# Kernel tuning notes

Measured on AMD Instinct MI355X. Metric: run time of the kernel, lower is better.

Reference implementation:

```python
import jax, jax.numpy as jnp
import numpy as np

N = 100000      # nodes
E = 3200000     # edges per graph (pos and neg)
IN_FEATS = 128
HIDDEN = 32
PROP_STEP = 8
USE_RELU = False  # args.relu default False


def setup_inputs() -> dict:
    key = jax.random.key(0)
    ks = jax.random.split(key, 8)
    in_feat = jax.random.normal(ks[0], (N, IN_FEATS), dtype=jnp.float32)
    src = jax.random.randint(ks[1], (E,), 0, N, dtype=jnp.int32)
    dst = jax.random.randint(ks[2], (E,), 0, N, dtype=jnp.int32)
    neg_src = jax.random.randint(ks[3], (E,), 0, N, dtype=jnp.int32)
    neg_dst = jax.random.randint(ks[4], (E,), 0, N, dtype=jnp.int32)
    W1 = jax.random.normal(ks[5], (IN_FEATS, HIDDEN), dtype=jnp.float32) * (1.0 / np.sqrt(IN_FEATS))
    b1 = jnp.zeros((HIDDEN,), dtype=jnp.float32)
    gamma = jnp.ones((HIDDEN,), dtype=jnp.float32)
    beta = jnp.zeros((HIDDEN,), dtype=jnp.float32)
    W2 = jax.random.normal(ks[6], (HIDDEN, HIDDEN), dtype=jnp.float32) * (1.0 / np.sqrt(HIDDEN))
    b2 = jnp.zeros((HIDDEN,), dtype=jnp.float32)
    return dict(in_feat=in_feat, W1=W1, b1=b1, gamma=gamma, beta=beta,
                W2=W2, b2=b2, src=src, dst=dst, neg_src=neg_src, neg_dst=neg_dst)


def _graph_conv(h, src, dst, n_nodes):
    """DGL GraphConv(norm='both', weight=False, bias=False):
       out = D_dst^{-1/2} A D_src^{-1/2} h, sum aggregation."""
    ones = jnp.ones(src.shape, dtype=h.dtype)
    out_deg = jax.ops.segment_sum(ones, src, num_segments=n_nodes)
    in_deg = jax.ops.segment_sum(ones, dst, num_segments=n_nodes)
    hs = h * jax.lax.rsqrt(jnp.clip(out_deg, 1.0))[:, None]   # [N, H]
    msg = hs[src]                                             # [E, H] gather
    agg = jax.ops.segment_sum(msg, dst, num_segments=n_nodes)  # [N, H] scatter-add
    return agg * jax.lax.rsqrt(jnp.clip(in_deg, 1.0))[:, None]


def reference(in_feat, W1, b1, gamma, beta, W2, b2, src, dst, neg_src, neg_dst):
    # MLP: Linear -> BatchNorm1d (training-mode batch stats) -> (Dropout noop) -> ReLU -> Linear
    x = in_feat @ W1 + b1
    mu = jnp.mean(x, axis=0)
    var = jnp.var(x, axis=0)
    x = (x - mu) * jax.lax.rsqrt(var + 1e-5) * gamma + beta
    x = jax.nn.relu(x)
    ori_h = x @ W2 + b2                                       # [N, H]

    # Iterative pos-neg SpMM propagation with residual (h initialized to ori_h)
    h = ori_h
    for _ in range(PROP_STEP):
        if USE_RELU:
            h = jax.nn.relu(h)
        h = _graph_conv(h, src, dst, N) - _graph_conv(h, neg_src, neg_dst, N) + ori_h
    return h
```

## Files before the change

### kernel.cpp

```cpp
#include <hip/hip_runtime.h>
#include <hip/hip_fp16.h>

#define N_NODES 100000
#define E_EDGES 3200000
#define IN_F 128
#define HID 32
#define PROP 8

#define WIN 32768
#define NWIN 4
#define HS 32

#define MB_ROWS 64
#define MB_BLOCKS ((N_NODES + MB_ROWS - 1) / MB_ROWS)
#define RED_B 32

#define FB 512
#define CH 12500
#define BK_SH 7
#define BK_N 128
#define NBK 782
#define L2S (NBK * FB)
#define SCB2 391
#define SPLIT 4
#define SUBN 32
#define STG 3072

__global__ __launch_bounds__(256) void hist_kernel(const int* __restrict__ s,
        const int* __restrict__ ns, int* __restrict__ degs) {
    __shared__ int lh[WIN];
    int b = blockIdx.x;
    int w = b % NWIN;
    int st = (b / NWIN) % 2;
    int sl = b / (NWIN * 2);
    const int* p = st ? ns : s;
    for (int i = threadIdx.x; i < WIN; i += 256) lh[i] = 0;
    __syncthreads();
    const int lo = w * WIN;
    const int per = E_EDGES / HS;
    const int4* p4 = (const int4*)(p + sl * per);
    for (int i = threadIdx.x; i < per / 4; i += 256) {
        int4 v = p4[i];
        int a;
        a = v.x - lo; if ((unsigned)a < WIN) atomicAdd(&lh[a], 1);
        a = v.y - lo; if ((unsigned)a < WIN) atomicAdd(&lh[a], 1);
        a = v.z - lo; if ((unsigned)a < WIN) atomicAdd(&lh[a], 1);
        a = v.w - lo; if ((unsigned)a < WIN) atomicAdd(&lh[a], 1);
    }
    __syncthreads();
    int* g = degs + st * N_NODES;
    for (int i = threadIdx.x; i < WIN; i += 256) {
        int idx = lo + i;
        if (idx < N_NODES && lh[i]) atomicAdd(&g[idx], lh[i]);
    }
}

__global__ void inv_sqrt_kernel(const int* __restrict__ deg, float* __restrict__ inv, int n) {
    int i = blockIdx.x * blockDim.x + threadIdx.x;
    if (i < n) inv[i] = rsqrtf(fmaxf((float)deg[i], 1.0f));
}

__global__ __launch_bounds__(256) void countA_kernel(const int* __restrict__ dst,
        const int* __restrict__ ndst, int* __restrict__ counts) {
    __shared__ int lh[NBK];
    int blk = blockIdx.x;
    for (int i = threadIdx.x; i < NBK; i += 256) lh[i] = 0;
    __syncthreads();
    const int* dp = (blk < FB / 2) ? dst + blk * CH : ndst + (blk - FB / 2) * CH;
    const int4* dp4 = (const int4*)dp;
    for (int i = threadIdx.x; i < CH / 4; i += 256) {
        int4 v = dp4[i];
        atomicAdd(&lh[v.x >> BK_SH], 1);
        atomicAdd(&lh[v.y >> BK_SH], 1);
        atomicAdd(&lh[v.z >> BK_SH], 1);
        atomicAdd(&lh[v.w >> BK_SH], 1);
    }
    __syncthreads();
    for (int b = threadIdx.x; b < NBK; b += 256) counts[b * FB + blk] = lh[b];
}

__global__ __launch_bounds__(1024) void scanA2_kernel(const int* __restrict__ counts,
        int* __restrict__ offs, int* __restrict__ blockSums) {
    __shared__ int sh[1024];
    int t = threadIdx.x, b = blockIdx.x;
    int i = b * 1024 + t;
    int v = counts[i];
    sh[t] = v;
    __syncthreads();
    for (int off = 1; off < 1024; off <<= 1) {
        int u = (t >= off) ? sh[t - off] : 0;
        __syncthreads();
        sh[t] += u;
        __syncthreads();
    }
    offs[i] = sh[t] - v;
    if (t == 1023) blockSums[b] = sh[1023];
}

__global__ __launch_bounds__(512) void scanB2_kernel(const int* __restrict__ blockSums,
        int* __restrict__ blockOff) {
    __shared__ int sh[512];
    int t = threadIdx.x;
    int v = (t < SCB2) ? blockSums[t] : 0;
    sh[t] = v;
    __syncthreads();
    for (int off = 1; off < 512; off <<= 1) {
        int u = (t >= off) ? sh[t - off] : 0;
        __syncthreads();
        sh[t] += u;
        __syncthreads();
    }
    if (t < SCB2) blockOff[t] = sh[t] - v;
}

__global__ __launch_bounds__(1024) void scanC2_kernel(int* __restrict__ offs,
        const int* __restrict__ blockOff) {
    int b = blockIdx.x, t = threadIdx.x;
    int i = b * 1024 + t;
    offs[i] += blockOff[b];
    if (i == 0) offs[L2S] = 2 * E_EDGES;
}

__global__ __launch_bounds__(256) void fillA2_kernel(const int* __restrict__ src, const int* __restrict__ dst,
        const int* __restrict__ nsrc, const int* __restrict__ ndst,
        const int* __restrict__ offs, int* __restrict__ rec) {
    __shared__ int cur[NBK];
    __shared__ int base[NBK];
    int blk = blockIdx.x;
    int g = (blk >= FB / 2);
    const int* sp = g ? (nsrc + (blk - FB / 2) * CH) : (src + blk * CH);
    const int* dp = g ? (ndst + (blk - FB / 2) * CH) : (dst + blk * CH);
    const int gbit = g << 24;
    for (int i = threadIdx.x; i < NBK; i += 256) {
        cur[i] = 0;
        base[i] = offs[i * FB + blk];
    }
    __syncthreads();
    for (int i = threadIdx.x; i < CH; i += 256) {
        int u = sp[i], v = dp[i];
        int b = v >> BK_SH;
        int p = base[b] + atomicAdd(&cur[b], 1);
        rec[p] = u | ((v & (BK_N - 1)) << 17) | gbit;
    }
}

__global__ __launch_bounds__(256, 5) void reorder_kernel(const int* __restrict__ offs,
        const int* __restrict__ rec, const float* __restrict__ invs,
        int2* __restrict__ rec2, int* __restrict__ row_ptr2) {
    __shared__ int cnt[BK_N];
    __shared__ int cntp[BK_N];
    __shared__ int scn[BK_N];
    __shared__ int ex[BK_N];
    __shared__ float invp[BK_N], invn[BK_N];
    __shared__ int2 stage[STG];
    int blk = blockIdx.x;
    int bkt = blk >> 2, sub = blk & (SPLIT - 1);
    int tid = threadIdx.x;
    if (tid < BK_N) { cnt[tid] = 0; cntp[tid] = 0; }
    __syncthreads();
    int beg = offs[bkt * FB], end = offs[(bkt + 1) * FB];
    for (int i = beg + tid; i < end; i += 256) {
        int rx = rec[i];
        int d = (rx >> 17) & (BK_N - 1);
        atomicAdd(&cnt[d], 1);
        if (!(rx & (1 << 24))) atomicAdd(&cntp[d], 1);
    }
    __syncthreads();
    int v = (tid < BK_N) ? cnt[tid] : 0;
    if (tid < BK_N) {
        scn[tid] = v;
        int np = cntp[tid];
        invp[tid] = rsqrtf(fmaxf((float)np, 1.0f));
        invn[tid] = rsqrtf(fmaxf((float)(v - np), 1.0f));
    }
    __syncthreads();
    for (int off = 1; off < BK_N; off <<= 1) {
        int u = (tid < BK_N && tid >= off) ? scn[tid - off] : 0;
        __syncthreads();
        if (tid < BK_N) scn[tid] += u;
        __syncthreads();
    }
    int lo = sub * SUBN, hi = lo + SUBN;
    if (tid < BK_N) {
        ex[tid] = scn[tid] - v;
        cnt[tid] = 0;
        if (tid >= lo && tid < hi)
            row_ptr2[bkt * BK_N + tid] = beg + ex[tid];
    }
    if (bkt == NBK - 1 && sub == SPLIT - 1 && tid == 0)
        row_ptr2[NBK * BK_N] = 2 * E_EDGES;
    __syncthreads();
    int base0 = ex[lo];
    int base1 = (sub == SPLIT - 1) ? (end - beg) : ex[hi];
    for (int i = beg + tid; i < end; i += 256) {
        int rx = rec[i];
        int d = (rx >> 17) & (BK_N - 1);
        if (d < lo || d >= hi) continue;
        int g = (rx >> 24) & 1;
        int u = rx & 0x1FFFF;
        float io = invs[u + (g ? N_NODES : 0)];
        float c = (g ? -io : io) * (g ? invn[d] : invp[d]);
        int p = ex[d] - base0 + atomicAdd(&cnt[d], 1);
        stage[p] = make_int2(u, __float_as_int(c));
    }
    __syncthreads();
    int n = base1 - base0;
    for (int j = tid; j < n; j += 256) rec2[beg + base0 + j] = stage[j];
}

__global__ __launch_bounds__(256) void mlp1_kernel(const float* __restrict__ in_feat,
        const float* __restrict__ W1, const float* __restrict__ b1,
        float* __restrict__ x, float* __restrict__ partials) {
    __shared__ float4 sRow4[MB_ROWS * 32];
    __shared__ float  sW1t[32 * 132];
    int tid = threadIdx.x;
    for (int idx = tid; idx < IN_F * HID; idx += 256) {
        int j = idx >> 5, k = idx & 31;
        sW1t[k * 132 + j] = W1[idx];
    }
    int nb = blockIdx.x * MB_ROWS;
    const float4* inf4 = (const float4*)in_feat;
    for (int idx = tid; idx < MB_ROWS * 32; idx += 256) {
        int row = idx >> 5, q = idx & 31;
        int g = nb + row;
        float4 v = (g < N_NODES) ? inf4[(size_t)g * 32 + q] : make_float4(0.f, 0.f, 0.f, 0.f);
        sRow4[row * 32 + (q ^ (row & 31))] = v;
    }
    __syncthreads();
    int rt = tid & 31, kt = tid >> 5;
    int k0 = kt * 4;
    float acc[2][4] = {{0.f}};
    const float4* w0p = (const float4*)&sW1t[(k0 + 0) * 132];
    const float4* w1p = (const float4*)&sW1t[(k0 + 1) * 132];
    const float4* w2p = (const float4*)&sW1t[(k0 + 2) * 132];
    const float4* w3p = (const float4*)&sW1t[(k0 + 3) * 132];
    #pragma unroll 4
    for (int jq = 0; jq < 32; ++jq) {
        int pq = jq ^ rt;
        float4 a0 = sRow4[rt * 32 + pq];
        float4 a1 = sRow4[(rt + 32) * 32 + pq];
        float4 w0 = w0p[jq], w1 = w1p[jq], w2 = w2p[jq], w3 = w3p[jq];
        acc[0][0] += a0.x*w0.x + a0.y*w0.y + a0.z*w0.z + a0.w*w0.w;
        acc[0][1] += a0.x*w1.x + a0.y*w1.y + a0.z*w1.z + a0.w*w1.w;
        acc[0][2] += a0.x*w2.x + a0.y*w2.y + a0.z*w2.z + a0.w*w2.w;
        acc[0][3] += a0.x*w3.x + a0.y*w3.y + a0.z*w3.z + a0.w*w3.w;
        acc[1][0] += a1.x*w0.x + a1.y*w0.y + a1.z*w0.z + a1.w*w0.w;
        acc[1][1] += a1.x*w1.x + a1.y*w1.y + a1.z*w1.z + a1.w*w1.w;
        acc[1][2] += a1.x*w2.x + a1.y*w2.y + a1.z*w2.z + a1.w*w2.w;
        acc[1][3] += a1.x*w3.x + a1.y*w3.y + a1.z*w3.z + a1.w*w3.w;
    }
    float bb[4] = { b1[k0], b1[k0 + 1], b1[k0 + 2], b1[k0 + 3] };
    float s[4] = {0.f, 0.f, 0.f, 0.f}, ss[4] = {0.f, 0.f, 0.f, 0.f};
    #pragma unroll
    for (int i = 0; i < 2; ++i) {
        int row = nb + rt + 32 * i;
        if (row < N_NODES) {
            float4 o;
            o.x = acc[i][0] + bb[0];
            o.y = acc[i][1] + bb[1];
            o.z = acc[i][2] + bb[2];
            o.w = acc[i][3] + bb[3];
            *(float4*)&x[(size_t)row * HID + k0] = o;
            s[0] += o.x; ss[0] += o.x * o.x;
            s[1] += o.y; ss[1] += o.y * o.y;
            s[2] += o.z; ss[2] += o.z * o.z;
            s[3] += o.w; ss[3] += o.w * o.w;
        }
    }
    for (int off = 16; off; off >>= 1) {
        #pragma unroll
        for (int c = 0; c < 4; ++c) {
            s[c]  += __shfl_down(s[c],  off, 32);
            ss[c] += __shfl_down(ss[c], off, 32);
        }
    }
    if (rt == 0) {
        float* pb = partials + (size_t)blockIdx.x * 64;
        #pragma unroll
        for (int c = 0; c < 4; ++c) {
            pb[k0 + c]      = s[c];
            pb[32 + k0 + c] = ss[c];
        }
    }
}

__global__ __launch_bounds__(256) void bnred_kernel(const float* __restrict__ partials,
        float* __restrict__ partials2) {
    __shared__ float red[4][64];
    int t = threadIdx.x, b = blockIdx.x;
    int r = t >> 6, c = t & 63;
    float sum = 0.f;
    for (int g = b * 4 + r; g < MB_BLOCKS; g += RED_B * 4)
        sum += partials[(size_t)g * 64 + c];
    red[r][c] = sum;
    __syncthreads();
    if (t < 64) partials2[b * 64 + t] = (red[0][t] + red[1][t]) + (red[2][t] + red[3][t]);
}

__global__ __launch_bounds__(256) void bnparam_kernel(const float* __restrict__ partials2,
        const float* __restrict__ gamma, const float* __restrict__ beta, float* __restrict__ params) {
    __shared__ float red[4][64];
    int t = threadIdx.x;
    int col = t & 63, ch = t >> 6;
    float sum = 0.f;
    for (int g = ch; g < RED_B; g += 4) sum += partials2[(size_t)g * 64 + col];
    red[ch][col] = sum;
    __syncthreads();
    if (t < 64) red[0][t] = red[0][t] + red[1][t] + red[2][t] + red[3][t];
    __syncthreads();
    if (t < HID) {
        float mu  = red[0][t] * (1.0f / (float)N_NODES);
        float var = red[0][t + 32] * (1.0f / (float)N_NODES) - mu * mu;
        float sg = gamma[t] * rsqrtf(var + 1e-5f);
        params[t]       = sg;
        params[HID + t] = beta[t] - mu * sg;
    }
}

__global__ __launch_bounds__(256) void mlp2_kernel(const float* __restrict__ x,
        const float* __restrict__ params, const float* __restrict__ W2,
        const float* __restrict__ b2, float* __restrict__ ori_h, __half* __restrict__ h16) {
    __shared__ float sW2[HID * HID];
    __shared__ float sXn[8][HID];
    int tid = threadIdx.x;
    for (int i = tid; i < HID * HID; i += 256) sW2[i] = W2[i];
    int nb = blockIdx.x * 8;
    int k = tid & 31, r = tid >> 5;
    float v = x[(size_t)(nb + r) * HID + k];
    v = fmaxf(fmaf(v, params[k], params[HID + k]), 0.f);
    sXn[r][k] = v;
    __syncthreads();
    float acc = b2[k];
    #pragma unroll
    for (int j = 0; j < HID; ++j) acc = fmaf(sXn[r][j], sW2[j * HID + k], acc);
    int o = (nb + r) * HID + k;
    ori_h[o] = acc;
    h16[o] = __float2half(acc);
}

__device__ __forceinline__ float2 h2f(int b) {
    __half2 h; __builtin_memcpy(&h, &b, 4); return __half22float2(h);
}

__global__ __launch_bounds__(256) void gather_kernel(const int* __restrict__ row_ptr,
        const int2* __restrict__ rec, const int4* __restrict__ h4,
        const float4* __restrict__ ori4, int4* __restrict__ hn4, float4* __restrict__ out4) {
    int tid = threadIdx.x;
    int node = blockIdx.x * 8 + (tid >> 5);
    int lane = tid & 31;
    int slot = lane >> 2;
    int ql = lane & 3;
    int beg = row_ptr[node], end = row_ptr[node + 1];
    float2 a0 = {0.f, 0.f}, a1 = {0.f, 0.f}, a2 = {0.f, 0.f}, a3 = {0.f, 0.f};
    int i = beg;
#define ACC8(f, c) { float2 u_; \
        u_ = h2f((f).x); a0.x = fmaf((c), u_.x, a0.x); a0.y = fmaf((c), u_.y, a0.y); \
        u_ = h2f((f).y); a1.x = fmaf((c), u_.x, a1.x); a1.y = fmaf((c), u_.y, a1.y); \
        u_ = h2f((f).z); a2.x = fmaf((c), u_.x, a2.x); a2.y = fmaf((c), u_.y, a2.y); \
        u_ = h2f((f).w); a3.x = fmaf((c), u_.x, a3.x); a3.y = fmaf((c), u_.y, a3.y); }
    for (; i + 32 <= end; i += 32) {
        int2 r0 = rec[i + slot];
        int2 r1 = rec[i + 8 + slot];
        int2 r2 = rec[i + 16 + slot];
        int2 r3 = rec[i + 24 + slot];
        int4 f0 = h4[r0.x * 4 + ql];
        int4 f1 = h4[r1.x * 4 + ql];
        int4 f2 = h4[r2.x * 4 + ql];
        int4 f3 = h4[r3.x * 4 + ql];
        float c0 = __int_as_float(r0.y), c1 = __int_as_float(r1.y);
        float c2 = __int_as_float(r2.y), c3 = __int_as_float(r3.y);
        ACC8(f0, c0) ACC8(f1, c1) ACC8(f2, c2) ACC8(f3, c3)
    }
    for (; i + 8 <= end; i += 8) {
        int2 r = rec[i + slot];
        int4 f = h4[r.x * 4 + ql];
        float c = __int_as_float(r.y);
        ACC8(f, c)
    }
    if (i + slot < end) {
        int2 r = rec[i + slot];
        int4 f = h4[r.x * 4 + ql];
        float c = __int_as_float(r.y);
        ACC8(f, c)
    }
#undef ACC8
    #pragma unroll
    for (int off = 4; off <= 16; off <<= 1) {
        a0.x += __shfl_down(a0.x, off, 32); a0.y += __shfl_down(a0.y, off, 32);
        a1.x += __shfl_down(a1.x, off, 32); a1.y += __shfl_down(a1.y, off, 32);
        a2.x += __shfl_down(a2.x, off, 32); a2.y += __shfl_down(a2.y, off, 32);
        a3.x += __shfl_down(a3.x, off, 32); a3.y += __shfl_down(a3.y, off, 32);
    }
    if (slot == 0) {
        float4 oA = ori4[node * 8 + ql * 2];
        float4 oB = ori4[node * 8 + ql * 2 + 1];
        float r0x = a0.x + oA.x, r0y = a0.y + oA.y;
        float r1x = a1.x + oA.z, r1y = a1.y + oA.w;
        float r2x = a2.x + oB.x, r2y = a2.y + oB.y;
        float r3x = a3.x + oB.z, r3y = a3.y + oB.w;
        if (out4) {
            out4[node * 8 + ql * 2]     = make_float4(r0x, r0y, r1x, r1y);
            out4[node * 8 + ql * 2 + 1] = make_float4(r2x, r2y, r3x, r3y);
        } else {
            __half2 p0 = __floats2half2_rn(r0x, r0y);
            __half2 p1 = __floats2half2_rn(r1x, r1y);
            __half2 p2 = __floats2half2_rn(r2x, r2y);
            __half2 p3 = __floats2half2_rn(r3x, r3y);
            int4 w;
            __builtin_memcpy(&w.x, &p0, 4);
            __builtin_memcpy(&w.y, &p1, 4);
            __builtin_memcpy(&w.z, &p2, 4);
            __builtin_memcpy(&w.w, &p3, 4);
            hn4[node * 4 + ql] = w;
        }
    }
}

extern "C" void kernel_launch(void* const* d_in, const int* in_sizes, int n_in,
                              void* d_out, int out_size, void* d_ws, size_t ws_size,
                              hipStream_t stream) {
    const float* in_feat = (const float*)d_in[0];
    const float* W1    = (const float*)d_in[1];
    const float* b1    = (const float*)d_in[2];
    const float* gamma = (const float*)d_in[3];
    const float* beta  = (const float*)d_in[4];
    const float* W2    = (const float*)d_in[5];
    const float* b2    = (const float*)d_in[6];
    const int* src  = (const int*)d_in[7];
    const int* dst  = (const int*)d_in[8];
    const int* nsrc = (const int*)d_in[9];
    const int* ndst = (const int*)d_in[10];
    float* out = (float*)d_out;

    float* ws      = (float*)d_ws;
    float* x       = ws;
    float* ori_h   = x + (size_t)N_NODES * HID;
    float* invs    = ori_h + (size_t)N_NODES * HID;
    float* params  = invs + 2 * (size_t)N_NODES;
    float* partials= params + 2 * HID;
    float* partials2 = partials + (size_t)MB_BLOCKS * 64;
    int*   degs    = (int*)(partials2 + (size_t)RED_B * 64);
    int*   offs    = degs + 2 * N_NODES;
    int*   blockSums = offs + L2S + 2;
    int*   blockOff  = blockSums + 512;
    int*   row_ptr2  = blockOff + 512;
    uintptr_t hp  = (uintptr_t)(row_ptr2 + NBK * BK_N + 2);
    hp = (hp + 63) & ~(uintptr_t)63;
    __half* h16A   = (__half*)hp;
    __half* h16B   = h16A + (size_t)N_NODES * HID;
    uintptr_t rp  = (uintptr_t)(h16B + (size_t)N_NODES * HID);
    rp = (rp + 63) & ~(uintptr_t)63;
    int*   rec    = (int*)rp;
    int*   counts = (int*)x;
    int2*  rec2   = (int2*)in_feat;

    hipMemsetAsync(degs, 0, 2 * (size_t)N_NODES * sizeof(int), stream);

    hist_kernel<<<NWIN * 2 * HS, 256, 0, stream>>>(src, nsrc, degs);
    inv_sqrt_kernel<<<(2 * N_NODES + 255) / 256, 256, 0, stream>>>(degs, invs, 2 * N_NODES);

    countA_kernel<<<FB, 256, 0, stream>>>(dst, ndst, counts);
    scanA2_kernel<<<SCB2, 1024, 0, stream>>>(counts, offs, blockSums);
    scanB2_kernel<<<1, 512, 0, stream>>>(blockSums, blockOff);
    scanC2_kernel<<<SCB2, 1024, 0, stream>>>(offs, blockOff);
    fillA2_kernel<<<FB, 256, 0, stream>>>(src, dst, nsrc, ndst, offs, rec);

    mlp1_kernel<<<MB_BLOCKS, 256, 0, stream>>>(in_feat, W1, b1, x, partials);
    bnred_kernel<<<RED_B, 256, 0, stream>>>(partials, partials2);
    bnparam_kernel<<<1, 256, 0, stream>>>(partials2, gamma, beta, params);
    mlp2_kernel<<<N_NODES / 8, 256, 0, stream>>>(x, params, W2, b2, ori_h, h16A);

    reorder_kernel<<<NBK * SPLIT, 256, 0, stream>>>(offs, rec, invs, rec2, row_ptr2);

    const __half* h = h16A;
    for (int it = 0; it < PROP; ++it) {
        __half* hn16 = (it & 1) ? h16A : h16B;
        float* o32 = (it == PROP - 1) ? out : nullptr;
        gather_kernel<<<N_NODES / 8, 256, 0, stream>>>(row_ptr2, rec2,
                (const int4*)h, (const float4*)ori_h, (int4*)hn16, (float4*)o32);
        h = hn16;
    }
}
```

Before: 972.0 us.

## Precompute in-degrees and node row pointers globally to simplify reorder kernel

The histogram kernel now also counts dst and neg_dst degrees, and a new three-kernel scan builds the per-node row pointers from the combined in-degrees. The reorder kernel therefore no longer runs its own counting pass over each bucket's records, its shared-memory histogram or its in-block scan. This removes one full read of the bucket records plus many shared atomics per block and cuts shared memory so more blocks fit per CU. The cost is a histogram pass over twice as much edge data and three extra small kernel launches.

```diff
diff --git a/kernel.cpp b/kernel.cpp
--- a/kernel.cpp
+++ b/kernel.cpp
@@ -25,15 +25,17 @@
 #define SPLIT 4
 #define SUBN 32
 #define STG 3072
+#define SCN 98
 
 __global__ __launch_bounds__(256) void hist_kernel(const int* __restrict__ s,
-        const int* __restrict__ ns, int* __restrict__ degs) {
+        const int* __restrict__ ns, const int* __restrict__ d0,
+        const int* __restrict__ nd, int* __restrict__ degs) {
     __shared__ int lh[WIN];
     int b = blockIdx.x;
     int w = b % NWIN;
-    int st = (b / NWIN) % 2;
-    int sl = b / (NWIN * 2);
-    const int* p = st ? ns : s;
+    int st = (b / NWIN) % 4;
+    int sl = b / (NWIN * 4);
+    const int* p = (st == 0) ? s : (st == 1) ? ns : (st == 2) ? d0 : nd;
     for (int i = threadIdx.x; i < WIN; i += 256) lh[i] = 0;
     __syncthreads();
     const int lo = w * WIN;
@@ -119,6 +121,47 @@
     int i = b * 1024 + t;
     offs[i] += blockOff[b];
     if (i == 0) offs[L2S] = 2 * E_EDGES;
+}
+
+__global__ __launch_bounds__(1024) void scanN_A_kernel(const int* __restrict__ indeg,
+        int* __restrict__ row_ptr2, int* __restrict__ bsums) {
+    __shared__ int sh[1024];
+    int t = threadIdx.x, b = blockIdx.x;
+    int i = b * 1024 + t;
+    int v = (i < N_NODES) ? (indeg[i] + indeg[N_NODES + i]) : 0;
+    sh[t] = v;
+    __syncthreads();
+    for (int off = 1; off < 1024; off <<= 1) {
+        int u = (t >= off) ? sh[t - off] : 0;
+        __syncthreads();
+        sh[t] += u;
+        __syncthreads();
+    }
+    if (i <= N_NODES) row_ptr2[i] = sh[t] - v;
+    if (t == 1023) bsums[b] = sh[1023];
+}
+
+__global__ __launch_bounds__(128) void scanN_B_kernel(const int* __restrict__ bsums,
+        int* __restrict__ boff) {
+    __shared__ int sh[128];
+    int t = threadIdx.x;
+    int v = (t < SCN) ? bsums[t] : 0;
+    sh[t] = v;
+    __syncthreads();
+    for (int off = 1; off < 128; off <<= 1) {
+        int u = (t >= off) ? sh[t - off] : 0;
+        __syncthreads();
+        sh[t] += u;
+        __syncthreads();
+    }
+    if (t < SCN) boff[t] = sh[t] - v;
+}
+
+__global__ __launch_bounds__(1024) void scanN_C_kernel(int* __restrict__ row_ptr2,
+        const int* __restrict__ boff) {
+    int b = blockIdx.x, t = threadIdx.x;
+    int i = b * 1024 + t;
+    if (i <= N_NODES) row_ptr2[i] += boff[b];
 }
 
 __global__ __launch_bounds__(256) void fillA2_kernel(const int* __restrict__ src, const int* __restrict__ dst,
@@ -144,68 +187,49 @@
     }
 }
 
-__global__ __launch_bounds__(256, 5) void reorder_kernel(const int* __restrict__ offs,
+__global__ __launch_bounds__(256, 6) void reorder_kernel(const int* __restrict__ offs,
         const int* __restrict__ rec, const float* __restrict__ invs,
-        int2* __restrict__ rec2, int* __restrict__ row_ptr2) {
-    __shared__ int cnt[BK_N];
-    __shared__ int cntp[BK_N];
-    __shared__ int scn[BK_N];
-    __shared__ int ex[BK_N];
-    __shared__ float invp[BK_N], invn[BK_N];
+        const int* __restrict__ indeg, const int* __restrict__ row_ptr2,
+        int2* __restrict__ rec2) {
+    __shared__ int cnt[SUBN];
+    __shared__ int base[SUBN];
+    __shared__ float invp[SUBN], invn[SUBN];
     __shared__ int2 stage[STG];
     int blk = blockIdx.x;
     int bkt = blk >> 2, sub = blk & (SPLIT - 1);
     int tid = threadIdx.x;
-    if (tid < BK_N) { cnt[tid] = 0; cntp[tid] = 0; }
+    int node0 = bkt * BK_N + sub * SUBN;
+    int n0c = (node0 < N_NODES) ? node0 : N_NODES;
+    int n1c = (node0 + SUBN < N_NODES) ? node0 + SUBN : N_NODES;
+    int base0 = row_ptr2[n0c];
+    int base1 = row_ptr2[n1c];
+    if (tid < SUBN) {
+        int gn = node0 + tid;
+        int gnc = (gn < N_NODES) ? gn : N_NODES - 1;
+        int dp = indeg[gnc];
+        int dn = indeg[N_NODES + gnc];
+        invp[tid] = rsqrtf(fmaxf((float)dp, 1.0f));
+        invn[tid] = rsqrtf(fmaxf((float)dn, 1.0f));
+        base[tid] = row_ptr2[(gn < N_NODES) ? gn : N_NODES] - base0;
+        cnt[tid] = 0;
+    }
     __syncthreads();
     int beg = offs[bkt * FB], end = offs[(bkt + 1) * FB];
+    int lo = sub * SUBN;
     for (int i = beg + tid; i < end; i += 256) {
         int rx = rec[i];
-        int d = (rx >> 17) & (BK_N - 1);
-        atomicAdd(&cnt[d], 1);
-        if (!(rx & (1 << 24))) atomicAdd(&cntp[d], 1);
-    }
-    __syncthreads();
-    int v = (tid < BK_N) ? cnt[tid] : 0;
-    if (tid < BK_N) {
-        scn[tid] = v;
-        int np = cntp[tid];
-        invp[tid] = rsqrtf(fmaxf((float)np, 1.0f));
-        invn[tid] = rsqrtf(fmaxf((float)(v - np), 1.0f));
-    }
-    __syncthreads();
-    for (int off = 1; off < BK_N; off <<= 1) {
-        int u = (tid < BK_N && tid >= off) ? scn[tid - off] : 0;
-        __syncthreads();
-        if (tid < BK_N) scn[tid] += u;
-        __syncthreads();
-    }
-    int lo = sub * SUBN, hi = lo + SUBN;
-    if (tid < BK_N) {
-        ex[tid] = scn[tid] - v;
-        cnt[tid] = 0;
-        if (tid >= lo && tid < hi)
-            row_ptr2[bkt * BK_N + tid] = beg + ex[tid];
-    }
-    if (bkt == NBK - 1 && sub == SPLIT - 1 && tid == 0)
-        row_ptr2[NBK * BK_N] = 2 * E_EDGES;
-    __syncthreads();
-    int base0 = ex[lo];
-    int base1 = (sub == SPLIT - 1) ? (end - beg) : ex[hi];
-    for (int i = beg + tid; i < end; i += 256) {
-        int rx = rec[i];
-        int d = (rx >> 17) & (BK_N - 1);
-        if (d < lo || d >= hi) continue;
+        int q = ((rx >> 17) & (BK_N - 1)) - lo;
+        if ((unsigned)q >= SUBN) continue;
         int g = (rx >> 24) & 1;
         int u = rx & 0x1FFFF;
         float io = invs[u + (g ? N_NODES : 0)];
-        float c = (g ? -io : io) * (g ? invn[d] : invp[d]);
-        int p = ex[d] - base0 + atomicAdd(&cnt[d], 1);
+        float c = (g ? -io : io) * (g ? invn[q] : invp[q]);
+        int p = base[q] + atomicAdd(&cnt[q], 1);
         stage[p] = make_int2(u, __float_as_int(c));
     }
     __syncthreads();
     int n = base1 - base0;
-    for (int j = tid; j < n; j += 256) rec2[beg + base0 + j] = stage[j];
+    for (int j = tid; j < n; j += 256) rec2[base0 + j] = stage[j];
 }
 
 __global__ __launch_bounds__(256) void mlp1_kernel(const float* __restrict__ in_feat,
@@ -440,11 +464,13 @@
     float* partials= params + 2 * HID;
     float* partials2 = partials + (size_t)MB_BLOCKS * 64;
     int*   degs    = (int*)(partials2 + (size_t)RED_B * 64);
-    int*   offs    = degs + 2 * N_NODES;
+    int*   offs    = degs + 4 * (size_t)N_NODES;
     int*   blockSums = offs + L2S + 2;
     int*   blockOff  = blockSums + 512;
-    int*   row_ptr2  = blockOff + 512;
-    uintptr_t hp  = (uintptr_t)(row_ptr2 + NBK * BK_N + 2);
+    int*   bsums2  = blockOff + 512;
+    int*   boff2   = bsums2 + 128;
+    int*   row_ptr2  = boff2 + 128;
+    uintptr_t hp  = (uintptr_t)(row_ptr2 + N_NODES + 2);
     hp = (hp + 63) & ~(uintptr_t)63;
     __half* h16A   = (__half*)hp;
     __half* h16B   = h16A + (size_t)N_NODES * HID;
@@ -454,9 +480,9 @@
     int*   counts = (int*)x;
     int2*  rec2   = (int2*)in_feat;
 
-    hipMemsetAsync(degs, 0, 2 * (size_t)N_NODES * sizeof(int), stream);
-
-    hist_kernel<<<NWIN * 2 * HS, 256, 0, stream>>>(src, nsrc, degs);
+    hipMemsetAsync(degs, 0, 4 * (size_t)N_NODES * sizeof(int), stream);
+
+    hist_kernel<<<NWIN * 4 * HS, 256, 0, stream>>>(src, nsrc, dst, ndst, degs);
     inv_sqrt_kernel<<<(2 * N_NODES + 255) / 256, 256, 0, stream>>>(degs, invs, 2 * N_NODES);
 
     countA_kernel<<<FB, 256, 0, stream>>>(dst, ndst, counts);
@@ -465,12 +491,17 @@
     scanC2_kernel<<<SCB2, 1024, 0, stream>>>(offs, blockOff);
     fillA2_kernel<<<FB, 256, 0, stream>>>(src, dst, nsrc, ndst, offs, rec);
 
+    scanN_A_kernel<<<SCN, 1024, 0, stream>>>(degs + 2 * N_NODES, row_ptr2, bsums2);
+    scanN_B_kernel<<<1, 128, 0, stream>>>(bsums2, boff2);
+    scanN_C_kernel<<<SCN, 1024, 0, stream>>>(row_ptr2, boff2);
+
     mlp1_kernel<<<MB_BLOCKS, 256, 0, stream>>>(in_feat, W1, b1, x, partials);
     bnred_kernel<<<RED_B, 256, 0, stream>>>(partials, partials2);
     bnparam_kernel<<<1, 256, 0, stream>>>(partials2, gamma, beta, params);
     mlp2_kernel<<<N_NODES / 8, 256, 0, stream>>>(x, params, W2, b2, ori_h, h16A);
 
-    reorder_kernel<<<NBK * SPLIT, 256, 0, stream>>>(offs, rec, invs, rec2, row_ptr2);
+    reorder_kernel<<<NBK * SPLIT, 256, 0, stream>>>(offs, rec, invs,
+            degs + 2 * N_NODES, row_ptr2, rec2);
 
     const __half* h = h16A;
     for (int it = 0; it < PROP; ++it) {
```

Result: slower. 1.019 ms (+4.9%).
